# Performance work log

Hardware: AMD Instinct MI355X
Metric: run time of the kernel (lower is better)

Reference implementation:

```python
import jax, jax.numpy as jnp
import numpy as np

B, S, D, H = 1, 2048, 1024, 16
HD = D // H
S_SLOPE = 10.0      # soft_thres_layer s
C_MASK = -10000.0   # soft_thres_layer c == masked_bias
ALPHA = 0.0         # config.threshold
W_STD = 0.02        # GPT2 init std for weights


def setup_inputs() -> dict:
    key = jax.random.key(0)
    k1, k2, k3 = jax.random.split(key, 3)
    return {
        "hidden_states": jax.random.normal(k1, (B, S, D), dtype=jnp.float32),
        "c_attn_w": jax.random.normal(k2, (D, 3 * D), dtype=jnp.float32) * W_STD,
        "c_attn_b": jnp.zeros((3 * D,), dtype=jnp.float32),
        "c_proj_w": jax.random.normal(k3, (D, D), dtype=jnp.float32) * W_STD,
        "c_proj_b": jnp.zeros((D,), dtype=jnp.float32),
    }


def reference(hidden_states, c_attn_w, c_attn_b, c_proj_w, c_proj_b):
    # Conv1D: x @ w + b (GPT2 convention: weight is [in, out])
    qkv = hidden_states @ c_attn_w + c_attn_b            # [B,S,3D]
    q, k, v = jnp.split(qkv, 3, axis=-1)

    def split_heads(x):
        return x.reshape(B, S, H, HD).transpose(0, 2, 1, 3)  # [B,H,S,hd]

    q, k, v = split_heads(q), split_heads(k), split_heads(v)

    # prun path: NO 1/sqrt(d) scaling (skipped when self.prun is True)
    w = jnp.einsum("bhqd,bhkd->bhqk", q, k)              # [B,H,S,S]

    causal = jnp.tril(jnp.ones((S, S), dtype=bool))[None, None]
    w = jnp.where(causal, w, C_MASK)

    # soft-threshold pruning: smoothly pushes scores below alpha toward c=-10000
    w = C_MASK + (w - C_MASK) * jax.nn.sigmoid(S_SLOPE * (w - ALPHA))

    a = jax.nn.softmax(w, axis=-1)                        # attn_dropout = identity (eval)
    out = jnp.einsum("bhqk,bhkd->bhqd", a, v)             # [B,H,S,hd]
    out = out.transpose(0, 2, 1, 3).reshape(B, S, D)      # merge heads
    return out @ c_proj_w + c_proj_b                      # resid_dropout = identity
```

## Files before the change

kernel.cpp:

```cpp
#include <hip/hip_runtime.h>


#define S_LEN 2048
#define DM    1024
#define NH    16
#define HD    64
#define NQKV  3072
#define SLOPE 10.0f
#define CMASK -10000.0f

typedef short s16x4 __attribute__((ext_vector_type(4)));
typedef short s16x8 __attribute__((ext_vector_type(8)));
typedef float f32x4 __attribute__((ext_vector_type(4)));

#define MFMA16(a,b,c) __builtin_amdgcn_mfma_f32_16x16x32_bf16(a,b,c,0,0,0)
#define GLDS16(g,l) __builtin_amdgcn_global_load_lds( \
    (const __attribute__((address_space(1))) void*)(g), \
    (__attribute__((address_space(3))) void*)(l), 16, 0, 0)

__device__ __forceinline__ short f2bf(float f){
    unsigned u = __float_as_uint(f);
    u += 0x7fffu + ((u >> 16) & 1u);
    return (short)(u >> 16);
}
struct bfpair { short hi, lo; };
__device__ __forceinline__ bfpair split_bf(float x){
    bfpair r; r.hi = f2bf(x);
    float fh = __uint_as_float(((unsigned)(unsigned short)r.hi) << 16);
    r.lo = f2bf(x - fh);
    return r;
}

template<int ROWS>
__device__ __forceinline__ void stage_tile(const short* gbase, int rstride,
                                           short* lds, int tid){
    const int lane = tid & 63, wid = tid >> 6;
#pragma unroll
    for (int it = 0; it < ROWS/32; ++it){
        int s = it*256 + wid*64 + lane;
        int row = s >> 3, grp = s & 7;
        const short* src = gbase + (size_t)row*rstride + ((grp ^ (row & 7)) << 3);
        GLDS16(src, lds + (size_t)(it*256 + wid*64)*8);
    }
}
__device__ __forceinline__ s16x8 frag(const short* lds, int row, int kg){
    return *(const s16x8*)&lds[row*64 + ((kg ^ (row & 7)) << 3)];
}

template<bool WSPLIT, bool QKV>
__global__ __launch_bounds__(256)
void gemm_kern(const short* __restrict__ Ahg, const short* __restrict__ Alg,
               const short* __restrict__ Bhg, const short* __restrict__ Blg,
               const float* __restrict__ bias,
               short* __restrict__ o0h, short* __restrict__ o0l,
               short* __restrict__ o1h, short* __restrict__ o1l,
               short* __restrict__ o2,  float* __restrict__ oproj)
{
    __shared__ __align__(16) short Ah_s[128*64];
    __shared__ __align__(16) short Al_s[128*64];
    __shared__ __align__(16) short Bh_s[128*64];
    __shared__ __align__(16) short Bl_s[WSPLIT ? 128*64 : 8];

    const int tid = threadIdx.x, lane = tid & 63, wid = tid >> 6;
    const int lr = lane & 15, lg = lane >> 4;
    const int brow = blockIdx.y*128, bcol = blockIdx.x*128;
    const int wm = (wid >> 1)*64, wn = (wid & 1)*64;

    f32x4 acc[4][4];
#pragma unroll
    for (int m = 0; m < 4; ++m)
#pragma unroll
        for (int n = 0; n < 4; ++n) acc[m][n] = (f32x4){0.f,0.f,0.f,0.f};

    for (int k0 = 0; k0 < DM; k0 += 64){
        stage_tile<128>(Ahg + (size_t)brow*DM + k0, DM, Ah_s, tid);
        stage_tile<128>(Alg + (size_t)brow*DM + k0, DM, Al_s, tid);
        stage_tile<128>(Bhg + (size_t)bcol*DM + k0, DM, Bh_s, tid);
        if constexpr (WSPLIT)
            stage_tile<128>(Blg + (size_t)bcol*DM + k0, DM, Bl_s, tid);
        __syncthreads();
#pragma unroll
        for (int kc = 0; kc < 2; ++kc){
            s16x8 ah[4], al[4], bh[4], bl[4];
#pragma unroll
            for (int m = 0; m < 4; ++m){
                ah[m] = frag(Ah_s, wm + m*16 + lr, kc*4 + lg);
                al[m] = frag(Al_s, wm + m*16 + lr, kc*4 + lg);
            }
#pragma unroll
            for (int n = 0; n < 4; ++n){
                bh[n] = frag(Bh_s, wn + n*16 + lr, kc*4 + lg);
                if constexpr (WSPLIT)
                    bl[n] = frag(Bl_s, wn + n*16 + lr, kc*4 + lg);
            }
#pragma unroll
            for (int m = 0; m < 4; ++m)
#pragma unroll
                for (int n = 0; n < 4; ++n){
                    acc[m][n] = MFMA16(ah[m], bh[n], acc[m][n]);
                    if constexpr (WSPLIT)
                        acc[m][n] = MFMA16(ah[m], bl[n], acc[m][n]);
                    acc[m][n] = MFMA16(al[m], bh[n], acc[m][n]);
                }
        }
        __syncthreads();
    }

    const int sec = bcol >> 10;
#pragma unroll
    for (int m = 0; m < 4; ++m)
#pragma unroll
        for (int n = 0; n < 4; ++n){
            int row  = brow + wm + m*16 + lg*4;
            int gcol = bcol + wn + n*16 + lr;
            float bv = bias[gcol];
#pragma unroll
            for (int v = 0; v < 4; ++v){
                float val = acc[m][n][v] + bv;
                if constexpr (QKV){
                    int col1 = gcol & 1023;
                    size_t o = (size_t)(row + v)*DM + col1;
                    if (sec == 0){ bfpair p = split_bf(val); o0h[o] = p.hi; o0l[o] = p.lo; }
                    else if (sec == 1){ bfpair p = split_bf(val); o1h[o] = p.hi; o1l[o] = p.lo; }
                    else { o2[o] = f2bf(val); }
                } else {
                    oproj[(size_t)(row + v)*DM + gcol] = val;
                }
            }
        }
}

__global__ __launch_bounds__(256)
void split_f32(const float* __restrict__ x, short* __restrict__ h,
               short* __restrict__ l, int n4)
{
    int i = blockIdx.x*256 + threadIdx.x;
    if (i >= n4) return;
    float4 v = *(const float4*)&x[(size_t)i*4];
    bfpair a = split_bf(v.x), b = split_bf(v.y), c = split_bf(v.z), d = split_bf(v.w);
    s16x4 hv, lv;
    hv.x = a.hi; hv.y = b.hi; hv.z = c.hi; hv.w = d.hi;
    lv.x = a.lo; lv.y = b.lo; lv.z = c.lo; lv.w = d.lo;
    *(s16x4*)&h[(size_t)i*4] = hv;
    *(s16x4*)&l[(size_t)i*4] = lv;
}

template<bool SPL>
__global__ __launch_bounds__(256)
void wtrans(const float* __restrict__ W, int N, short* __restrict__ Th,
            short* __restrict__ Tl)
{
    __shared__ float t[64][65];
    const int tid = threadIdx.x;
    const int tn = blockIdx.x*64, tk = blockIdx.y*64;
#pragma unroll
    for (int it = 0; it < 4; ++it){
        int idx = tid + it*256;
        int r = idx >> 4, c4 = (idx & 15)*4;
        float4 v = *(const float4*)&W[(size_t)(tk + r)*N + tn + c4];
        t[r][c4] = v.x; t[r][c4+1] = v.y; t[r][c4+2] = v.z; t[r][c4+3] = v.w;
    }
    __syncthreads();
#pragma unroll
    for (int it = 0; it < 4; ++it){
        int idx = tid + it*256;
        int n = idx >> 4, c4 = (idx & 15)*4;
        s16x4 hv, lv;
#pragma unroll
        for (int j = 0; j < 4; ++j){
            bfpair p = split_bf(t[c4+j][n]);
            hv[j] = p.hi; lv[j] = p.lo;
        }
        *(s16x4*)&Th[(size_t)(tn + n)*DM + tk + c4] = hv;
        if constexpr (SPL) *(s16x4*)&Tl[(size_t)(tn + n)*DM + tk + c4] = lv;
    }
}

__global__ __launch_bounds__(256)
void vtrans(const short* __restrict__ Vb, short* __restrict__ Vt)
{
    __shared__ short t[64][66];
    const int tid = threadIdx.x;
    const int td = blockIdx.x*64, ts = blockIdx.y*64;
#pragma unroll
    for (int it = 0; it < 4; ++it){
        int idx = tid + it*256;
        int r = idx >> 4, c4 = (idx & 15)*4;
        s16x4 v = *(const s16x4*)&Vb[(size_t)(ts + r)*DM + td + c4];
        t[r][c4] = v.x; t[r][c4+1] = v.y; t[r][c4+2] = v.z; t[r][c4+3] = v.w;
    }
    __syncthreads();
#pragma unroll
    for (int it = 0; it < 4; ++it){
        int idx = tid + it*256;
        int n = idx >> 4, c4 = (idx & 15)*4;
        s16x4 o;
#pragma unroll
        for (int j = 0; j < 4; ++j) o[j] = t[c4+j][n];
        *(s16x4*)&Vt[(size_t)(td + n)*S_LEN + ts + c4] = o;
    }
}

__global__ __launch_bounds__(256)
void attn_fwd(const short* __restrict__ Qh, const short* __restrict__ Ql,
              const short* __restrict__ Kh, const short* __restrict__ Kl,
              const short* __restrict__ Vt,
              short* __restrict__ Oh, short* __restrict__ Ol)
{
    __shared__ __align__(16) short qh_s[64*64], ql_s[64*64];
    __shared__ __align__(16) short kh_s[64*64], kl_s[64*64];
    __shared__ __align__(16) short vt_s[64*64];
    __shared__ __align__(16) short Ps[4][16*72];

    const int qb = blockIdx.x, h = blockIdx.y;
    const int tid = threadIdx.x, lane = tid & 63, wid = tid >> 6;
    const int lr = lane & 15, lg = lane >> 4;

    stage_tile<64>(Qh + (size_t)(qb*64)*DM + h*HD, DM, qh_s, tid);
    stage_tile<64>(Ql + (size_t)(qb*64)*DM + h*HD, DM, ql_s, tid);
    __syncthreads();

    s16x8 aqh[2], aql[2];
#pragma unroll
    for (int kc = 0; kc < 2; ++kc){
        aqh[kc] = frag(qh_s, wid*16 + lr, kc*4 + lg);
        aql[kc] = frag(ql_s, wid*16 + lr, kc*4 + lg);
    }
    __syncthreads();

    float m_run[4], l_run[4];
    f32x4 acc_o[4];
#pragma unroll
    for (int v = 0; v < 4; ++v){ m_run[v] = -1e30f; l_run[v] = 0.f; }
#pragma unroll
    for (int n = 0; n < 4; ++n) acc_o[n] = (f32x4){0.f,0.f,0.f,0.f};

    const int qrow = qb*64 + wid*16 + lg*4;

    for (int kvb = 0; kvb < S_LEN/64; ++kvb){
        stage_tile<64>(Kh + (size_t)(kvb*64)*DM + h*HD, DM, kh_s, tid);
        stage_tile<64>(Kl + (size_t)(kvb*64)*DM + h*HD, DM, kl_s, tid);
        stage_tile<64>(Vt + (size_t)(h*HD)*S_LEN + kvb*64, S_LEN, vt_s, tid);
        __syncthreads();

        f32x4 sc[4];
#pragma unroll
        for (int n = 0; n < 4; ++n) sc[n] = (f32x4){0.f,0.f,0.f,0.f};
#pragma unroll
        for (int kc = 0; kc < 2; ++kc)
#pragma unroll
            for (int n = 0; n < 4; ++n){
                s16x8 bkh = frag(kh_s, n*16 + lr, kc*4 + lg);
                s16x8 bkl = frag(kl_s, n*16 + lr, kc*4 + lg);
                sc[n] = MFMA16(aqh[kc], bkh, sc[n]);
                sc[n] = MFMA16(aqh[kc], bkl, sc[n]);
                sc[n] = MFMA16(aql[kc], bkh, sc[n]);
            }

        float p[4][4], tmax[4];
#pragma unroll
        for (int v = 0; v < 4; ++v) tmax[v] = -1e30f;
#pragma unroll
        for (int n = 0; n < 4; ++n){
            int key = kvb*64 + n*16 + lr;
#pragma unroll
            for (int v = 0; v < 4; ++v){
                float w;
                if (key > qrow + v) w = CMASK;
                else {
                    float sv = sc[n][v];
                    float sig = 1.f / (1.f + __expf(-SLOPE*sv));
                    w = CMASK + (sv - CMASK)*sig;
                }
                p[n][v] = w;
                tmax[v] = fmaxf(tmax[v], w);
            }
        }
#pragma unroll
        for (int v = 0; v < 4; ++v)
#pragma unroll
            for (int msk = 1; msk < 16; msk <<= 1)
                tmax[v] = fmaxf(tmax[v], __shfl_xor(tmax[v], msk, 64));

        float scale[4], rsum[4];
#pragma unroll
        for (int v = 0; v < 4; ++v){
            float mn = fmaxf(m_run[v], tmax[v]);
            scale[v] = __expf(m_run[v] - mn);
            m_run[v] = mn;
            rsum[v] = 0.f;
        }
#pragma unroll
        for (int n = 0; n < 4; ++n)
#pragma unroll
            for (int v = 0; v < 4; ++v){
                float e = __expf(p[n][v] - m_run[v]);
                p[n][v] = e;
                rsum[v] += e;
            }
#pragma unroll
        for (int v = 0; v < 4; ++v){
#pragma unroll
            for (int msk = 1; msk < 16; msk <<= 1)
                rsum[v] += __shfl_xor(rsum[v], msk, 64);
            l_run[v] = l_run[v]*scale[v] + rsum[v];
        }
#pragma unroll
        for (int n = 0; n < 4; ++n)
#pragma unroll
            for (int v = 0; v < 4; ++v) acc_o[n][v] *= scale[v];

#pragma unroll
        for (int n = 0; n < 4; ++n)
#pragma unroll
            for (int v = 0; v < 4; ++v)
                Ps[wid][(lg*4 + v)*72 + 16*n + lr] = f2bf(p[n][v]);
        asm volatile("s_waitcnt lgkmcnt(0)" ::: "memory");

        s16x8 pa0 = *(const s16x8*)&Ps[wid][lr*72 + lg*8];
        s16x8 pa1 = *(const s16x8*)&Ps[wid][lr*72 + 32 + lg*8];
#pragma unroll
        for (int n = 0; n < 4; ++n){
            s16x8 bv0 = frag(vt_s, 16*n + lr, lg);
            s16x8 bv1 = frag(vt_s, 16*n + lr, 4 + lg);
            acc_o[n] = MFMA16(pa0, bv0, acc_o[n]);
            acc_o[n] = MFMA16(pa1, bv1, acc_o[n]);
        }

        int ok = (kvb >= qb);
#pragma unroll
        for (int v = 0; v < 4; ++v)
            ok = ok && (m_run[v] > CMASK + 100.f);
        if (__syncthreads_and(ok)) break;
    }

#pragma unroll
    for (int n = 0; n < 4; ++n)
#pragma unroll
        for (int v = 0; v < 4; ++v){
            int row = qrow + v;
            int col = h*HD + 16*n + lr;
            bfpair p = split_bf(acc_o[n][v] / l_run[v]);
            Oh[(size_t)row*DM + col] = p.hi;
            Ol[(size_t)row*DM + col] = p.lo;
        }
}

extern "C" void kernel_launch(void* const* d_in, const int* in_sizes, int n_in,
                              void* d_out, int out_size, void* d_ws, size_t ws_size,
                              hipStream_t stream)
{
    (void)in_sizes; (void)n_in; (void)out_size; (void)ws_size;
    const float* hs   = (const float*)d_in[0];
    const float* wqkv = (const float*)d_in[1];
    const float* bqkv = (const float*)d_in[2];
    const float* wprj = (const float*)d_in[3];
    const float* bprj = (const float*)d_in[4];

    char* p = (char*)d_ws;
    short* Ahg  = (short*)(p + (0ull  << 20));
    short* Alg  = (short*)(p + (4ull  << 20));
    short* WqTh = (short*)(p + (8ull  << 20));
    short* WqTl = (short*)(p + (14ull << 20));
    short* Qhg  = (short*)(p + (20ull << 20));
    short* Qlg  = (short*)(p + (24ull << 20));
    short* Khg  = (short*)(p + (28ull << 20));
    short* Klg  = (short*)(p + (32ull << 20));
    short* Vbg  = (short*)(p + (36ull << 20));
    short* Vtg  = (short*)(p + (40ull << 20));
    short* Oh = Ahg, * Ol = Alg;
    short* WpT = WqTh;

    split_f32<<<S_LEN*DM/4/256, 256, 0, stream>>>(hs, Ahg, Alg, S_LEN*DM/4);
    wtrans<true><<<dim3(NQKV/64, DM/64), 256, 0, stream>>>(wqkv, NQKV, WqTh, WqTl);

    gemm_kern<true, true><<<dim3(NQKV/128, S_LEN/128), 256, 0, stream>>>(
        Ahg, Alg, WqTh, WqTl, bqkv, Qhg, Qlg, Khg, Klg, Vbg, nullptr);

    wtrans<false><<<dim3(DM/64, DM/64), 256, 0, stream>>>(wprj, DM, WpT, nullptr);
    vtrans<<<dim3(DM/64, S_LEN/64), 256, 0, stream>>>(Vbg, Vtg);

    attn_fwd<<<dim3(S_LEN/64, NH), 256, 0, stream>>>(Qhg, Qlg, Khg, Klg, Vtg, Oh, Ol);

    gemm_kern<false, false><<<dim3(DM/128, S_LEN/128), 256, 0, stream>>>(
        Oh, Ol, WpT, nullptr, bprj, nullptr, nullptr, nullptr, nullptr, nullptr,
        (float*)d_out);
}
```

Before: 204.1 us.

## Shrink attention query tile to 32 rows, reorder blocks, skip mask off-diagonal

The attention kernel now processes 32 query rows per block with 128 threads instead of 64 rows with 256 threads, which doubles the grid and shortens the causal critical path per block. The block-to-query-tile mapping reverses order for alternating groups so long and short causal rows are interleaved across the grid. The causal mask check is applied only on diagonal tiles, and the early-exit condition uses the new diagonal index. The trade-off is that each K/V tile is now loaded by twice as many blocks, with fewer threads to issue those loads.

```diff
diff --git a/kernel.cpp b/kernel.cpp
--- a/kernel.cpp
+++ b/kernel.cpp
@@ -8,6 +8,7 @@
 #define NQKV  3072
 #define SLOPE 10.0f
 #define CMASK -10000.0f
+#define QROWS 32
 
 typedef short s16x4 __attribute__((ext_vector_type(4)));
 typedef short s16x8 __attribute__((ext_vector_type(8)));
@@ -31,16 +32,15 @@
     return r;
 }
 
-template<int ROWS>
+template<int ROWS, int THREADS>
 __device__ __forceinline__ void stage_tile(const short* gbase, int rstride,
                                            short* lds, int tid){
-    const int lane = tid & 63, wid = tid >> 6;
-#pragma unroll
-    for (int it = 0; it < ROWS/32; ++it){
-        int s = it*256 + wid*64 + lane;
+#pragma unroll
+    for (int it = 0; it < ROWS*8/THREADS; ++it){
+        int s = it*THREADS + tid;
         int row = s >> 3, grp = s & 7;
         const short* src = gbase + (size_t)row*rstride + ((grp ^ (row & 7)) << 3);
-        GLDS16(src, lds + (size_t)(it*256 + wid*64)*8);
+        GLDS16(src, lds + (size_t)s*8);
     }
 }
 __device__ __forceinline__ s16x8 frag(const short* lds, int row, int kg){
@@ -73,11 +73,11 @@
         for (int n = 0; n < 4; ++n) acc[m][n] = (f32x4){0.f,0.f,0.f,0.f};
 
     for (int k0 = 0; k0 < DM; k0 += 64){
-        stage_tile<128>(Ahg + (size_t)brow*DM + k0, DM, Ah_s, tid);
-        stage_tile<128>(Alg + (size_t)brow*DM + k0, DM, Al_s, tid);
-        stage_tile<128>(Bhg + (size_t)bcol*DM + k0, DM, Bh_s, tid);
+        stage_tile<128,256>(Ahg + (size_t)brow*DM + k0, DM, Ah_s, tid);
+        stage_tile<128,256>(Alg + (size_t)brow*DM + k0, DM, Al_s, tid);
+        stage_tile<128,256>(Bhg + (size_t)bcol*DM + k0, DM, Bh_s, tid);
         if constexpr (WSPLIT)
-            stage_tile<128>(Blg + (size_t)bcol*DM + k0, DM, Bl_s, tid);
+            stage_tile<128,256>(Blg + (size_t)bcol*DM + k0, DM, Bl_s, tid);
         __syncthreads();
 #pragma unroll
         for (int kc = 0; kc < 2; ++kc){
@@ -201,23 +201,27 @@
     }
 }
 
-__global__ __launch_bounds__(256)
+__global__ __launch_bounds__(128)
 void attn_fwd(const short* __restrict__ Qh, const short* __restrict__ Ql,
               const short* __restrict__ Kh, const short* __restrict__ Kl,
               const short* __restrict__ Vt,
               short* __restrict__ Oh, short* __restrict__ Ol)
 {
-    __shared__ __align__(16) short qh_s[64*64], ql_s[64*64];
+    __shared__ __align__(16) short qh_s[QROWS*64], ql_s[QROWS*64];
     __shared__ __align__(16) short kh_s[64*64], kl_s[64*64];
     __shared__ __align__(16) short vt_s[64*64];
-    __shared__ __align__(16) short Ps[4][16*72];
-
-    const int qb = blockIdx.x, h = blockIdx.y;
+    __shared__ __align__(16) short Ps[2][16*72];
+
+    const int bx = blockIdx.x, h = blockIdx.y;
+    const int lid = bx + (h << 6);
+    const int qt = ((lid >> 8) & 1) ? bx : (S_LEN/QROWS - 1) - bx;
+    const int diag = (qt*QROWS + QROWS - 1) >> 6;
+
     const int tid = threadIdx.x, lane = tid & 63, wid = tid >> 6;
     const int lr = lane & 15, lg = lane >> 4;
 
-    stage_tile<64>(Qh + (size_t)(qb*64)*DM + h*HD, DM, qh_s, tid);
-    stage_tile<64>(Ql + (size_t)(qb*64)*DM + h*HD, DM, ql_s, tid);
+    stage_tile<QROWS,128>(Qh + (size_t)(qt*QROWS)*DM + h*HD, DM, qh_s, tid);
+    stage_tile<QROWS,128>(Ql + (size_t)(qt*QROWS)*DM + h*HD, DM, ql_s, tid);
     __syncthreads();
 
     s16x8 aqh[2], aql[2];
@@ -226,7 +230,6 @@
         aqh[kc] = frag(qh_s, wid*16 + lr, kc*4 + lg);
         aql[kc] = frag(ql_s, wid*16 + lr, kc*4 + lg);
     }
-    __syncthreads();
 
     float m_run[4], l_run[4];
     f32x4 acc_o[4];
@@ -235,12 +238,12 @@
 #pragma unroll
     for (int n = 0; n < 4; ++n) acc_o[n] = (f32x4){0.f,0.f,0.f,0.f};
 
-    const int qrow = qb*64 + wid*16 + lg*4;
+    const int qrow = qt*QROWS + wid*16 + lg*4;
 
     for (int kvb = 0; kvb < S_LEN/64; ++kvb){
-        stage_tile<64>(Kh + (size_t)(kvb*64)*DM + h*HD, DM, kh_s, tid);
-        stage_tile<64>(Kl + (size_t)(kvb*64)*DM + h*HD, DM, kl_s, tid);
-        stage_tile<64>(Vt + (size_t)(h*HD)*S_LEN + kvb*64, S_LEN, vt_s, tid);
+        stage_tile<64,128>(Kh + (size_t)(kvb*64)*DM + h*HD, DM, kh_s, tid);
+        stage_tile<64,128>(Kl + (size_t)(kvb*64)*DM + h*HD, DM, kl_s, tid);
+        stage_tile<64,128>(Vt + (size_t)(h*HD)*S_LEN + kvb*64, S_LEN, vt_s, tid);
         __syncthreads();
 
         f32x4 sc[4];
@@ -260,21 +263,34 @@
         float p[4][4], tmax[4];
 #pragma unroll
         for (int v = 0; v < 4; ++v) tmax[v] = -1e30f;
-#pragma unroll
-        for (int n = 0; n < 4; ++n){
-            int key = kvb*64 + n*16 + lr;
-#pragma unroll
-            for (int v = 0; v < 4; ++v){
-                float w;
-                if (key > qrow + v) w = CMASK;
-                else {
+        if (kvb >= diag){
+#pragma unroll
+            for (int n = 0; n < 4; ++n){
+                int key = kvb*64 + n*16 + lr;
+#pragma unroll
+                for (int v = 0; v < 4; ++v){
+                    float w;
+                    if (key > qrow + v) w = CMASK;
+                    else {
+                        float sv = sc[n][v];
+                        float sig = 1.f / (1.f + __expf(-SLOPE*sv));
+                        w = CMASK + (sv - CMASK)*sig;
+                    }
+                    p[n][v] = w;
+                    tmax[v] = fmaxf(tmax[v], w);
+                }
+            }
+        } else {
+#pragma unroll
+            for (int n = 0; n < 4; ++n)
+#pragma unroll
+                for (int v = 0; v < 4; ++v){
                     float sv = sc[n][v];
                     float sig = 1.f / (1.f + __expf(-SLOPE*sv));
-                    w = CMASK + (sv - CMASK)*sig;
+                    float w = CMASK + (sv - CMASK)*sig;
+                    p[n][v] = w;
+                    tmax[v] = fmaxf(tmax[v], w);
                 }
-                p[n][v] = w;
-                tmax[v] = fmaxf(tmax[v], w);
-            }
         }
 #pragma unroll
         for (int v = 0; v < 4; ++v)
@@ -327,7 +343,7 @@
             acc_o[n] = MFMA16(pa1, bv1, acc_o[n]);
         }
 
-        int ok = (kvb >= qb);
+        int ok = (kvb >= diag);
 #pragma unroll
         for (int v = 0; v < 4; ++v)
             ok = ok && (m_run[v] > CMASK + 100.f);
@@ -380,7 +396,7 @@
     wtrans<false><<<dim3(DM/64, DM/64), 256, 0, stream>>>(wprj, DM, WpT, nullptr);
     vtrans<<<dim3(DM/64, S_LEN/64), 256, 0, stream>>>(Vbg, Vtg);
 
-    attn_fwd<<<dim3(S_LEN/64, NH), 256, 0, stream>>>(Qhg, Qlg, Khg, Klg, Vtg, Oh, Ol);
+    attn_fwd<<<dim3(S_LEN/QROWS, NH), 128, 0, stream>>>(Qhg, Qlg, Khg, Klg, Vtg, Oh, Ol);
 
     gemm_kern<false, false><<<dim3(DM/128, S_LEN/128), 256, 0, stream>>>(
         Oh, Ol, WpT, nullptr, bprj, nullptr, nullptr, nullptr, nullptr, nullptr,
```

After: 195.2 us. 1.05x faster.
